# Performance work log

Hardware: AMD Instinct MI355X
Metric: run time of the kernel (lower is better)

Reference implementation:

```python
import jax, jax.numpy as jnp
import numpy as np

B, N, P = 64, 800000, 128          # batch, total CpG features, n_pathways (capsules)
H1, H2, C = 256, 128, 32           # MLP hidden_topology and n_output
EPS = 1e-5                         # BatchNorm1d eps


def _xavier(key, fan_in, fan_out, shape):
    bound = np.sqrt(6.0 / (fan_in + fan_out))
    return jax.random.uniform(key, shape, jnp.float32, -bound, bound)


def setup_inputs() -> dict:
    key = jax.random.key(0)
    ks = jax.random.split(key, 10)
    x = jax.random.normal(ks[0], (B, N), jnp.float32)
    # idx: sorted pathway assignment, equal capsule sizes N//P (matches module_lens)
    idx = jnp.sort(jax.random.randint(ks[1], (N,), 0, P)).astype(jnp.int64)
    # SPWModulesLayer.weight: xavier_uniform on shape (1, N)
    w = _xavier(ks[2], N, 1, (N,))
    co_w = jax.random.uniform(ks[3], (P,), jnp.float32, 0.0, 4.0)  # CancelOut init
    bn0_g, bn0_b = jnp.ones(P, jnp.float32), jnp.zeros(P, jnp.float32)
    W1, b1 = _xavier(ks[4], P, H1, (P, H1)), jnp.zeros(H1, jnp.float32)
    bn1_g, bn1_b = jnp.ones(H1, jnp.float32), jnp.zeros(H1, jnp.float32)
    W2, b2 = _xavier(ks[5], H1, H2, (H1, H2)), jnp.zeros(H2, jnp.float32)
    bn2_g, bn2_b = jnp.ones(H2, jnp.float32), jnp.zeros(H2, jnp.float32)
    Wo, bo = _xavier(ks[6], H2, C, (H2, C)), jnp.zeros(C, jnp.float32)
    return {"x": x, "w": w, "co_w": co_w,
            "bn0_g": bn0_g, "bn0_b": bn0_b,
            "W1": W1, "b1": b1, "bn1_g": bn1_g, "bn1_b": bn1_b,
            "W2": W2, "b2": b2, "bn2_g": bn2_g, "bn2_b": bn2_b,
            "Wo": Wo, "bo": bo, "idx": idx}


def _bn(z, g, b):
    # BatchNorm1d in training mode: batch mean, biased variance
    m = jnp.mean(z, axis=0)
    v = jnp.mean((z - m) ** 2, axis=0)
    return (z - m) * jax.lax.rsqrt(v + EPS) * g + b


def reference(x, w, co_w, bn0_g, bn0_b, W1, b1, bn1_g, bn1_b,
              W2, b2, bn2_g, bn2_b, Wo, bo, idx):
    # --- SPWModulesLayer: weighted scatter_add over pathway index (last dim) ---
    WX = jnp.zeros((x.shape[0], P), x.dtype).at[:, idx].add(x * w)   # [B, P]
    Z = _bn(jax.nn.relu(WX), bn0_g, bn0_b)                           # ReLU + BN
    Z = Z * jax.nn.sigmoid(co_w)                                     # CancelOut
    # --- MLP head: Linear->ReLU->BN twice, then Linear->Softmax ---
    h = _bn(jax.nn.relu(Z @ W1 + b1), bn1_g, bn1_b)
    h = _bn(jax.nn.relu(h @ W2 + b2), bn2_g, bn2_b)
    y = jax.nn.softmax(h @ Wo + bo, axis=-1)
    return (y, Z)
```

## Files before the change

### kernel.cpp

```cpp
#include <hip/hip_runtime.h>
#include <hip/hip_bf16.h>

#define BB     64
#define NF4    200000
#define CHUNKS 3125
#define NP     128
#define NH1    256
#define NH2    128
#define NC     32
#define EPSV   1e-5f

typedef float fx4 __attribute__((ext_vector_type(4)));

#define AS_G __attribute__((address_space(1)))
#define AS_L __attribute__((address_space(3)))

__device__ __forceinline__ float dot4(fx4 a, fx4 b) {
    return fmaf(a[0], b[0], fmaf(a[1], b[1], fmaf(a[2], b[2], a[3] * b[3])));
}

__device__ __forceinline__ int bitrev3(int l) {
    return ((l & 1) << 2) | (l & 2) | ((l & 4) >> 2);
}

template <int C, int M>
__device__ __forceinline__ void red_step(float* v, int lane) {
    const bool hi = (lane & M) != 0;
    #pragma unroll
    for (int j = 0; j < C / 2; ++j) {
        float mine  = hi ? v[j + C / 2] : v[j];
        float other = hi ? v[j]         : v[j + C / 2];
        v[j] = mine + __shfl_xor(other, M);
    }
}

__device__ __forceinline__ float reduce8(float* acc, int lane) {
    red_step<8, 1>(acc, lane);
    red_step<4, 2>(acc, lane);
    red_step<2, 4>(acc, lane);
    float s = acc[0];
    s += __shfl_xor(s, 8);
    s += __shfl_xor(s, 16);
    s += __shfl_xor(s, 32);
    return s;
}

__global__ __launch_bounds__(128) void k_scatter(
    const float* __restrict__ x, const float* __restrict__ w,
    const int* __restrict__ idx, float* __restrict__ WX)
{
    __shared__ fx4 lds4[2 * 2 * 8 * 64];
    const int tid  = threadIdx.x;
    const int lane = tid & 63;
    const int q    = tid >> 6;
    const int ch   = blockIdx.x * 2 + q;
    if (ch >= CHUNKS) return;
    const int n4   = ch * 64 + lane;

    const fx4*  __restrict__ w4 = reinterpret_cast<const fx4*>(w);
    const int4* __restrict__ p4 = reinterpret_cast<const int4*>(idx);
    const fx4*  __restrict__ x4 = reinterpret_cast<const fx4*>(x);

    const fx4  wv = w4[n4];
    const int4 pv = p4[n4];
    const int  pLo = __builtin_amdgcn_readfirstlane(pv.x);
    const int  pHi = __shfl(pv.w, 63);
    const bool uniform = (pLo == pHi);

    fx4 wLo, wHi;
    wLo[0] = (pv.x == pLo) ? wv[0] : 0.f;  wHi[0] = (pv.x == pHi) ? wv[0] : 0.f;
    wLo[1] = (pv.y == pLo) ? wv[1] : 0.f;  wHi[1] = (pv.y == pHi) ? wv[1] : 0.f;
    wLo[2] = (pv.z == pLo) ? wv[2] : 0.f;  wHi[2] = (pv.z == pHi) ? wv[2] : 0.f;
    wLo[3] = (pv.w == pLo) ? wv[3] : 0.f;  wHi[3] = (pv.w == pHi) ? wv[3] : 0.f;

    fx4* const base = lds4 + q * (2 * 8 * 64);

    auto dma = [&](int o) {
        const int s = o & 1;
        #pragma unroll
        for (int i = 0; i < 8; ++i) {
            const float* gp = (const float*)(x4 + ((size_t)(o * 8 + i) * NF4 + n4));
            __builtin_amdgcn_global_load_lds((const AS_G float*)gp,
                                             (AS_L float*)(base + (s * 8 + i) * 64),
                                             16, 0, 0);
        }
    };

    dma(0); dma(1);

    #pragma unroll
    for (int o = 0; o < 8; ++o) {
        if (o == 0)      asm volatile("s_waitcnt vmcnt(8)" ::: "memory");
        else if (o < 7)  asm volatile("s_waitcnt vmcnt(9)" ::: "memory");
        else             asm volatile("s_waitcnt vmcnt(1)" ::: "memory");

        const int s = o & 1;
        fx4 xr[8];
        #pragma unroll
        for (int i = 0; i < 8; ++i) {
            const unsigned laddr =
                (unsigned)(size_t)(AS_L char*)(base + (s * 8 + i) * 64 + lane);
            asm volatile("ds_read_b128 %0, %1" : "=v"(xr[i]) : "v"(laddr));
        }
        asm volatile("s_waitcnt lgkmcnt(0)" ::: "memory");
        __builtin_amdgcn_sched_barrier(0);

        float acc[8], accH[8];
        #pragma unroll
        for (int i = 0; i < 8; ++i)
            acc[i] = dot4(xr[i], wLo);
        const float sLo = reduce8(acc, lane);
        float sHi = 0.f;
        if (!uniform) {
            #pragma unroll
            for (int i = 0; i < 8; ++i)
                accH[i] = dot4(xr[i], wHi);
            sHi = reduce8(accH, lane);
        }
        const int   b0  = o * 8;
        const float val = (lane < 8) ? sLo : sHi;
        const int   col = (lane < 8) ? pLo : pHi;
        const int   nl  = uniform ? 8 : 16;
        if (lane < nl)
            atomicAdd(&WX[(b0 + bitrev3(lane & 7)) * NP + col], val);

        __builtin_amdgcn_sched_barrier(0);
        if (o + 2 < 8) dma(o + 2);
        __builtin_amdgcn_sched_barrier(0);
    }
}

__global__ void k_zero(float* __restrict__ WX)
{
    const int i = blockIdx.x * 256 + threadIdx.x;
    if (i < BB * NP) WX[i] = 0.f;
}

__device__ __forceinline__ float bn_shfl(float a, float gj, float bj)
{
    float s = a, q = a * a;
    #pragma unroll
    for (int off = 32; off > 0; off >>= 1) {
        s += __shfl_xor(s, off);
        q += __shfl_xor(q, off);
    }
    const float m   = s * (1.f / BB);
    const float var = q * (1.f / BB) - m * m;
    return (a - m) * rsqrtf(var + EPSV) * gj + bj;
}

__global__ __launch_bounds__(256) void k_fc1z(
    const float* __restrict__ WX,   const float* __restrict__ co_w,
    const float* __restrict__ bn0g, const float* __restrict__ bn0b,
    const float* __restrict__ W1,   const float* __restrict__ b1,
    const float* __restrict__ bn1g, const float* __restrict__ bn1b,
    float* __restrict__ Zout, float* __restrict__ h1t)
{
    __shared__ float Zl[NP * 65];
    const int tid  = threadIdx.x;
    const int wv   = tid >> 6;
    const int lane = tid & 63;
    const int blk  = blockIdx.x;

    if (tid < NP) {
        const int p = tid;
        float sum = 0.f, sq = 0.f;
        #pragma unroll 8
        for (int b = 0; b < BB; ++b) {
            const float r = fmaxf(WX[b * NP + p], 0.f);
            sum += r; sq += r * r;
        }
        const float m   = sum * (1.f / BB);
        const float var = sq * (1.f / BB) - m * m;
        const float sc  = rsqrtf(var + EPSV) * bn0g[p];
        const float bt  = bn0b[p];
        const float sig = 1.f / (1.f + expf(-co_w[p]));
        #pragma unroll 8
        for (int b = 0; b < BB; ++b) {
            const float r = fmaxf(WX[b * NP + p], 0.f);
            const float z = ((r - m) * sc + bt) * sig;
            Zl[p * 65 + b] = z;
            if (blk == 0) Zout[b * NP + p] = z;
        }
    }
    __syncthreads();

    const int j = blk * 4 + wv;
    float acc = b1[j];
    #pragma unroll 8
    for (int k = 0; k < NP; ++k)
        acc = fmaf(Zl[k * 65 + lane], W1[k * NH1 + j], acc);
    h1t[j * BB + lane] = bn_shfl(fmaxf(acc, 0.f), bn1g[j], bn1b[j]);
}

template <int K, int NOUT>
__global__ void k_fc_bn_t(const float* __restrict__ in_t,
                          const float* __restrict__ W,
                          const float* __restrict__ bias,
                          const float* __restrict__ g,
                          const float* __restrict__ beta,
                          float* __restrict__ out_t)
{
    const int j = blockIdx.x;
    const int b = threadIdx.x;
    float acc = bias[j];
    #pragma unroll 8
    for (int k = 0; k < K; ++k)
        acc = fmaf(in_t[k * BB + b], W[k * NOUT + j], acc);
    out_t[j * BB + b] = bn_shfl(fmaxf(acc, 0.f), g[j], beta[j]);
}

__global__ void k_head(const float* __restrict__ h2t,
                       const float* __restrict__ Wo,
                       const float* __restrict__ bo,
                       float* __restrict__ y)
{
    const int b = blockIdx.x;
    const int c = threadIdx.x;
    float acc = bo[c];
    #pragma unroll 8
    for (int k = 0; k < NH2; ++k)
        acc = fmaf(h2t[k * BB + b], Wo[k * NC + c], acc);
    float mx = acc;
    #pragma unroll
    for (int off = 16; off > 0; off >>= 1)
        mx = fmaxf(mx, __shfl_xor(mx, off));
    const float e = expf(acc - mx);
    float s = e;
    #pragma unroll
    for (int off = 16; off > 0; off >>= 1)
        s += __shfl_xor(s, off);
    y[b * NC + c] = e / s;
}

extern "C" void kernel_launch(void* const* d_in, const int* in_sizes, int n_in,
                              void* d_out, int out_size, void* d_ws, size_t ws_size,
                              hipStream_t stream)
{
    const float* x    = (const float*)d_in[0];
    const float* w    = (const float*)d_in[1];
    const float* co_w = (const float*)d_in[2];
    const float* bn0g = (const float*)d_in[3];
    const float* bn0b = (const float*)d_in[4];
    const float* W1   = (const float*)d_in[5];
    const float* b1   = (const float*)d_in[6];
    const float* bn1g = (const float*)d_in[7];
    const float* bn1b = (const float*)d_in[8];
    const float* W2   = (const float*)d_in[9];
    const float* b2   = (const float*)d_in[10];
    const float* bn2g = (const float*)d_in[11];
    const float* bn2b = (const float*)d_in[12];
    const float* Wo   = (const float*)d_in[13];
    const float* bo   = (const float*)d_in[14];
    const int*   idx  = (const int*)d_in[15];

    float* out = (float*)d_out;
    float* y   = out;
    float* Z   = out + BB * NC;

    float* WX  = (float*)d_ws;
    float* h1t = WX + BB * NP;
    float* h2t = h1t + BB * NH1;

    k_zero<<<32, 256, 0, stream>>>(WX);
    k_scatter<<<(CHUNKS + 1) / 2, 128, 0, stream>>>(x, w, idx, WX);
    k_fc1z<<<64, 256, 0, stream>>>(WX, co_w, bn0g, bn0b,
                                   W1, b1, bn1g, bn1b, Z, h1t);
    k_fc_bn_t<NH1, NH2><<<NH2, BB, 0, stream>>>(h1t, W2, b2, bn2g, bn2b, h2t);
    k_head<<<BB, NC, 0, stream>>>(h2t, Wo, bo, y);
}
```

Baseline: 85.60 us.

## Transpose scatter reduction via padded LDS layout and defer atomics to end

The scatter kernel now runs one wave per block. It reads the staged x tile from LDS in a transposed pattern using padded rows, so each lane accumulates across features for a fixed batch row instead of doing a full cross-lane reduction per batch group. Per-batch-group shuffle reductions and per-iteration atomics are replaced by register accumulation over all 8 batch groups, followed by one butterfly reduction and a single atomic per lane at the end. Weights and indices are also staged through LDS. This cuts shuffle and atomic traffic, but adds more registers for the per-lane weight vectors and a serial wait on the weight/index load.

```diff
diff --git a/kernel.cpp b/kernel.cpp
--- a/kernel.cpp
+++ b/kernel.cpp
@@ -9,6 +9,8 @@
 #define NH2    128
 #define NC     32
 #define EPSV   1e-5f
+#define ROWPAD 1040
+#define SLOT   (8 * ROWPAD)
 
 typedef float fx4 __attribute__((ext_vector_type(4)));
 
@@ -34,99 +36,108 @@
     }
 }
 
-__device__ __forceinline__ float reduce8(float* acc, int lane) {
-    red_step<8, 1>(acc, lane);
-    red_step<4, 2>(acc, lane);
-    red_step<2, 4>(acc, lane);
-    float s = acc[0];
-    s += __shfl_xor(s, 8);
-    s += __shfl_xor(s, 16);
-    s += __shfl_xor(s, 32);
-    return s;
-}
-
-__global__ __launch_bounds__(128) void k_scatter(
+__global__ __launch_bounds__(64) void k_scatter(
     const float* __restrict__ x, const float* __restrict__ w,
     const int* __restrict__ idx, float* __restrict__ WX)
 {
-    __shared__ fx4 lds4[2 * 2 * 8 * 64];
-    const int tid  = threadIdx.x;
-    const int lane = tid & 63;
-    const int q    = tid >> 6;
-    const int ch   = blockIdx.x * 2 + q;
-    if (ch >= CHUNKS) return;
+    __shared__ char lds[2 * SLOT + 2048];
+    const int lane = threadIdx.x;
+    const int ch   = blockIdx.x;
     const int n4   = ch * 64 + lane;
 
-    const fx4*  __restrict__ w4 = reinterpret_cast<const fx4*>(w);
+    const fx4* __restrict__ x4 = reinterpret_cast<const fx4*>(x);
+    const fx4* __restrict__ w4 = reinterpret_cast<const fx4*>(w);
     const int4* __restrict__ p4 = reinterpret_cast<const int4*>(idx);
-    const fx4*  __restrict__ x4 = reinterpret_cast<const fx4*>(x);
-
-    const fx4  wv = w4[n4];
-    const int4 pv = p4[n4];
-    const int  pLo = __builtin_amdgcn_readfirstlane(pv.x);
-    const int  pHi = __shfl(pv.w, 63);
+
+    const int  pLo = idx[ch * 256];
+    const int  pHi = idx[ch * 256 + 255];
     const bool uniform = (pLo == pHi);
 
-    fx4 wLo, wHi;
-    wLo[0] = (pv.x == pLo) ? wv[0] : 0.f;  wHi[0] = (pv.x == pHi) ? wv[0] : 0.f;
-    wLo[1] = (pv.y == pLo) ? wv[1] : 0.f;  wHi[1] = (pv.y == pHi) ? wv[1] : 0.f;
-    wLo[2] = (pv.z == pLo) ? wv[2] : 0.f;  wHi[2] = (pv.z == pHi) ? wv[2] : 0.f;
-    wLo[3] = (pv.w == pLo) ? wv[3] : 0.f;  wHi[3] = (pv.w == pHi) ? wv[3] : 0.f;
-
-    fx4* const base = lds4 + q * (2 * 8 * 64);
+    char* const wbuf = lds + 2 * SLOT;
+    char* const pbuf = lds + 2 * SLOT + 1024;
+
+    __builtin_amdgcn_global_load_lds((const AS_G float*)(w4 + n4),
+                                     (AS_L float*)wbuf, 16, 0, 0);
+    __builtin_amdgcn_global_load_lds((const AS_G float*)(p4 + n4),
+                                     (AS_L float*)pbuf, 16, 0, 0);
+    asm volatile("s_waitcnt vmcnt(0)" ::: "memory");
+
+    fx4 wLo[8], wHi[8];
+    #pragma unroll
+    for (int j = 0; j < 8; ++j) {
+        const int c = (lane >> 3) + 8 * j;
+        const fx4  wj = *reinterpret_cast<const fx4*>(wbuf + c * 16);
+        const int4 pj = *reinterpret_cast<const int4*>(pbuf + c * 16);
+        wLo[j][0] = (pj.x == pLo) ? wj[0] : 0.f;
+        wLo[j][1] = (pj.y == pLo) ? wj[1] : 0.f;
+        wLo[j][2] = (pj.z == pLo) ? wj[2] : 0.f;
+        wLo[j][3] = (pj.w == pLo) ? wj[3] : 0.f;
+        if (!uniform) {
+            wHi[j][0] = (pj.x == pHi) ? wj[0] : 0.f;
+            wHi[j][1] = (pj.y == pHi) ? wj[1] : 0.f;
+            wHi[j][2] = (pj.z == pHi) ? wj[2] : 0.f;
+            wHi[j][3] = (pj.w == pHi) ? wj[3] : 0.f;
+        }
+    }
 
     auto dma = [&](int o) {
-        const int s = o & 1;
+        char* const sb = lds + (o & 1) * SLOT;
         #pragma unroll
         for (int i = 0; i < 8; ++i) {
             const float* gp = (const float*)(x4 + ((size_t)(o * 8 + i) * NF4 + n4));
             __builtin_amdgcn_global_load_lds((const AS_G float*)gp,
-                                             (AS_L float*)(base + (s * 8 + i) * 64),
+                                             (AS_L float*)(sb + i * ROWPAD),
                                              16, 0, 0);
         }
     };
 
     dma(0); dma(1);
 
+    float acc[8], accH[8];
     #pragma unroll
     for (int o = 0; o < 8; ++o) {
-        if (o == 0)      asm volatile("s_waitcnt vmcnt(8)" ::: "memory");
-        else if (o < 7)  asm volatile("s_waitcnt vmcnt(9)" ::: "memory");
-        else             asm volatile("s_waitcnt vmcnt(1)" ::: "memory");
-
-        const int s = o & 1;
+        if (o < 7) asm volatile("s_waitcnt vmcnt(8)" ::: "memory");
+        else       asm volatile("s_waitcnt vmcnt(0)" ::: "memory");
+
+        char* const sb = lds + (o & 1) * SLOT;
         fx4 xr[8];
         #pragma unroll
-        for (int i = 0; i < 8; ++i) {
-            const unsigned laddr =
-                (unsigned)(size_t)(AS_L char*)(base + (s * 8 + i) * 64 + lane);
-            asm volatile("ds_read_b128 %0, %1" : "=v"(xr[i]) : "v"(laddr));
+        for (int j = 0; j < 8; ++j) {
+            const unsigned laddr = (unsigned)(size_t)(AS_L char*)
+                (sb + (lane & 7) * ROWPAD + (((lane >> 3) + 8 * j) * 16));
+            asm volatile("ds_read_b128 %0, %1" : "=v"(xr[j]) : "v"(laddr));
         }
         asm volatile("s_waitcnt lgkmcnt(0)" ::: "memory");
         __builtin_amdgcn_sched_barrier(0);
 
-        float acc[8], accH[8];
+        float t[8];
         #pragma unroll
-        for (int i = 0; i < 8; ++i)
-            acc[i] = dot4(xr[i], wLo);
-        const float sLo = reduce8(acc, lane);
-        float sHi = 0.f;
+        for (int j = 0; j < 8; ++j)
+            t[j] = dot4(xr[j], wLo[j]);
+        acc[o] = ((t[0] + t[1]) + (t[2] + t[3])) + ((t[4] + t[5]) + (t[6] + t[7]));
         if (!uniform) {
+            float th[8];
             #pragma unroll
-            for (int i = 0; i < 8; ++i)
-                accH[i] = dot4(xr[i], wHi);
-            sHi = reduce8(accH, lane);
-        }
-        const int   b0  = o * 8;
-        const float val = (lane < 8) ? sLo : sHi;
-        const int   col = (lane < 8) ? pLo : pHi;
-        const int   nl  = uniform ? 8 : 16;
-        if (lane < nl)
-            atomicAdd(&WX[(b0 + bitrev3(lane & 7)) * NP + col], val);
+            for (int j = 0; j < 8; ++j)
+                th[j] = dot4(xr[j], wHi[j]);
+            accH[o] = ((th[0] + th[1]) + (th[2] + th[3])) + ((th[4] + th[5]) + (th[6] + th[7]));
+        }
 
         __builtin_amdgcn_sched_barrier(0);
-        if (o + 2 < 8) dma(o + 2);
+        if (o < 6) dma(o + 2);
         __builtin_amdgcn_sched_barrier(0);
+    }
+
+    const int batch = bitrev3(lane >> 3) * 8 + (lane & 7);
+    red_step<8, 8>(acc, lane);
+    red_step<4, 16>(acc, lane);
+    red_step<2, 32>(acc, lane);
+    atomicAdd(&WX[batch * NP + pLo], acc[0]);
+    if (!uniform) {
+        red_step<8, 8>(accH, lane);
+        red_step<4, 16>(accH, lane);
+        red_step<2, 32>(accH, lane);
+        atomicAdd(&WX[batch * NP + pHi], accH[0]);
     }
 }
 
@@ -263,7 +274,7 @@
     float* h2t = h1t + BB * NH1;
 
     k_zero<<<32, 256, 0, stream>>>(WX);
-    k_scatter<<<(CHUNKS + 1) / 2, 128, 0, stream>>>(x, w, idx, WX);
+    k_scatter<<<CHUNKS, 64, 0, stream>>>(x, w, idx, WX);
     k_fc1z<<<64, 256, 0, stream>>>(WX, co_w, bn0g, bn0b,
                                    W1, b1, bn1g, bn1b, Z, h1t);
     k_fc_bn_t<NH1, NH2><<<NH2, BB, 0, stream>>>(h1t, W2, b2, bn2g, bn2b, h2t);
```

After: 88.23 us. 1.03x slower.
